# Performance work log

Measured on AMD Instinct MI355X. Metric: run time of the kernel, lower is better.

Reference implementation:

```python
import jax, jax.numpy as jnp
import numpy as np

B, S, D, H = 4, 2048, 1024, 16
HD = D // H
DFF = 4 * D
EPS = 1e-5


def gelu_tanh(x):
    c = jnp.sqrt(jnp.asarray(2.0 / jnp.pi, x.dtype))
    return 0.5 * x * (1.0 + jnp.tanh(c * (x + 0.044715 * x ** 3)))


def layernorm(x, scale, shift):
    mean = jnp.mean(x, axis=-1, keepdims=True)
    var = jnp.var(x, axis=-1, keepdims=True)  # unbiased=False
    return scale * (x - mean) * jax.lax.rsqrt(var + EPS) + shift


def setup_inputs() -> dict:
    key = jax.random.key(0)
    ks = jax.random.split(key, 12)
    s_in = 1.0 / np.sqrt(D)
    s_ff = 1.0 / np.sqrt(DFF)
    return {
        "x": jax.random.normal(ks[0], (B, S, D), jnp.float32),
        "Wq": jax.random.uniform(ks[1], (D, D), jnp.float32, -s_in, s_in),
        "Wk": jax.random.uniform(ks[2], (D, D), jnp.float32, -s_in, s_in),
        "Wv": jax.random.uniform(ks[3], (D, D), jnp.float32, -s_in, s_in),
        "Wo": jax.random.uniform(ks[4], (D, D), jnp.float32, -s_in, s_in),
        "bo": jax.random.uniform(ks[5], (D,), jnp.float32, -s_in, s_in),
        "W1": jax.random.uniform(ks[6], (D, DFF), jnp.float32, -s_in, s_in),
        "b1": jax.random.uniform(ks[7], (DFF,), jnp.float32, -s_in, s_in),
        "W2": jax.random.uniform(ks[8], (DFF, D), jnp.float32, -s_ff, s_ff),
        "b2": jax.random.uniform(ks[9], (D,), jnp.float32, -s_ff, s_ff),
        "ln1_scale": jnp.ones((D,), jnp.float32),
        "ln1_shift": jnp.zeros((D,), jnp.float32),
        "ln2_scale": jnp.ones((D,), jnp.float32),
        "ln2_shift": jnp.zeros((D,), jnp.float32),
    }


def reference(x, Wq, Wk, Wv, Wo, bo, W1, b1, W2, b2,
              ln1_scale, ln1_shift, ln2_scale, ln2_shift):
    # --- pre-LN causal MHA ---
    h = layernorm(x, ln1_scale, ln1_shift)
    q = (h @ Wq).reshape(B, S, H, HD).transpose(0, 2, 1, 3)  # [B,H,S,hd]
    k = (h @ Wk).reshape(B, S, H, HD).transpose(0, 2, 1, 3)
    v = (h @ Wv).reshape(B, S, H, HD).transpose(0, 2, 1, 3)
    scores = jnp.einsum('bhqd,bhkd->bhqk', q, k)
    causal = jnp.tril(jnp.ones((S, S), bool))  # mask strict upper triangle
    scores = jnp.where(causal, scores, -jnp.inf)
    attn = jax.nn.softmax(scores / np.sqrt(HD), axis=-1)
    ctx = jnp.einsum('bhqk,bhkd->bhqd', attn, v)
    ctx = ctx.transpose(0, 2, 1, 3).reshape(B, S, D)
    x = x + (ctx @ Wo + bo)
    # --- FFN ---
    h = layernorm(x, ln2_scale, ln2_shift)
    h = gelu_tanh(h @ W1 + b1) @ W2 + b2
    return x + h
```

## Files before the change

### kernel.cpp

```cpp
#include <hip/hip_runtime.h>
#include <math.h>

#define S_LEN  2048
#define DMODEL 1024
#define NHEAD  16
#define BATCH  4
#define NROWS  (BATCH*S_LEN)
#define DFF    4096
#define QKV_LD 3072

typedef __attribute__((ext_vector_type(4))) unsigned short us4;
typedef __attribute__((ext_vector_type(8))) unsigned short us8;
typedef __attribute__((ext_vector_type(8))) __bf16 bf16x8;
typedef __attribute__((ext_vector_type(4))) float f32x4;

#if __has_builtin(__builtin_amdgcn_exp2f)
#define EXP2(x) __builtin_amdgcn_exp2f(x)
#else
#define EXP2(x) exp2f(x)
#endif
#if __has_builtin(__builtin_amdgcn_rcpf)
#define RCP(x) __builtin_amdgcn_rcpf(x)
#else
#define RCP(x) (1.0f/(x))
#endif

static __device__ __forceinline__ unsigned short f2bf(float f) {
  __bf16 b = (__bf16)f;
  return __builtin_bit_cast(unsigned short, b);
}
#define GLD16(gp, lp) __builtin_amdgcn_global_load_lds( \
    (const __attribute__((address_space(1))) unsigned int*)(gp), \
    (__attribute__((address_space(3))) unsigned int*)(lp), 16, 0, 0)

static __device__ __forceinline__ int xcd_swz(int bid, int nwg) {
  int q = nwg >> 3;
  return (bid & 7) * q + (bid >> 3);
}

__global__ __launch_bounds__(256) void ln_kernel(
    const float* __restrict__ x, const float* __restrict__ scale,
    const float* __restrict__ shift, unsigned short* __restrict__ out)
{
  const int row = blockIdx.x, tid = threadIdx.x;
  const int lane = tid & 63, wave = tid >> 6;
  const float* xr = x + (size_t)row * DMODEL;
  f32x4 v = *(const f32x4*)&xr[tid * 4];
  float s  = v[0]+v[1]+v[2]+v[3];
  float s2 = v[0]*v[0]+v[1]*v[1]+v[2]*v[2]+v[3]*v[3];
  #pragma unroll
  for (int m = 1; m < 64; m <<= 1) { s += __shfl_xor(s, m); s2 += __shfl_xor(s2, m); }
  __shared__ float red[8];
  if (lane == 0) { red[wave] = s; red[4 + wave] = s2; }
  __syncthreads();
  s  = red[0]+red[1]+red[2]+red[3];
  s2 = red[4]+red[5]+red[6]+red[7];
  float mean = s * (1.0f/DMODEL);
  float var  = s2 * (1.0f/DMODEL) - mean*mean;
  float rstd = rsqrtf(var + 1e-5f);
  us4 o;
  #pragma unroll
  for (int j = 0; j < 4; j++) {
    float val = (v[j]-mean)*rstd*scale[tid*4+j] + shift[tid*4+j];
    o[j] = f2bf(val);
  }
  *(us4*)&out[(size_t)row*DMODEL + tid*4] = o;
}

__global__ __launch_bounds__(256) void wtrans_all(
    const float* __restrict__ Wq, const float* __restrict__ Wk,
    const float* __restrict__ Wv, const float* __restrict__ Wo,
    const float* __restrict__ W1, const float* __restrict__ W2,
    unsigned short* __restrict__ wqkvt, unsigned short* __restrict__ wot,
    unsigned short* __restrict__ w1t, unsigned short* __restrict__ w2t,
    float sclq)
{
  __shared__ unsigned short tile[64][72];
  const int bid = blockIdx.x, tid = threadIdx.x;
  const float* W; unsigned short* Wt; int K, N, sub; float scl = 1.0f;
  if (bid < 1024) {
    int wsel = bid >> 8; sub = bid & 255; K = 1024; N = 1024;
    W  = (wsel == 0) ? Wq : (wsel == 1) ? Wk : (wsel == 2) ? Wv : Wo;
    Wt = (wsel == 0) ? wqkvt : (wsel == 1) ? wqkvt + 1024*1024
       : (wsel == 2) ? wqkvt + 2048*1024 : wot;
    if (wsel == 0) scl = sclq;
  } else if (bid < 2048) { sub = bid - 1024; K = 1024; N = 4096; W = W1; Wt = w1t; }
  else                   { sub = bid - 2048; K = 4096; N = 1024; W = W2; Wt = w2t; }
  const int nbn = N >> 6;
  const int kt = sub / nbn, nt = sub % nbn;
  int r = tid >> 2, c0 = (tid & 3) << 4;
  const float* src = W + (size_t)(kt*64 + r)*N + nt*64 + c0;
  #pragma unroll
  for (int j = 0; j < 16; j += 4) {
    f32x4 f = *(const f32x4*)&src[j];
    tile[r][c0+j+0] = f2bf(f[0]*scl); tile[r][c0+j+1] = f2bf(f[1]*scl);
    tile[r][c0+j+2] = f2bf(f[2]*scl); tile[r][c0+j+3] = f2bf(f[3]*scl);
  }
  __syncthreads();
  int n = tid >> 2, k0 = (tid & 3) << 4;
  us8 o0, o1;
  #pragma unroll
  for (int j = 0; j < 8; j++) { o0[j] = tile[k0+j][n]; o1[j] = tile[k0+8+j][n]; }
  unsigned short* dst = Wt + (size_t)(nt*64 + n)*K + kt*64 + k0;
  *(us8*)&dst[0] = o0;
  *(us8*)&dst[8] = o1;
}

__global__ __launch_bounds__(256) void vtrans(
    const unsigned short* __restrict__ v, unsigned short* __restrict__ vt)
{
  __shared__ unsigned short tile[64][72];
  const int tid = threadIdx.x;
  const int bh = blockIdx.x >> 5, st = blockIdx.x & 31;
  const int b = bh >> 4, h = bh & 15;
  int r = tid >> 2, c0 = (tid & 3) << 4;
  const unsigned short* src = v + (size_t)(b*S_LEN + st*64 + r)*QKV_LD + h*64 + c0;
  *(us8*)&tile[r][c0]   = *(const us8*)&src[0];
  *(us8*)&tile[r][c0+8] = *(const us8*)&src[8];
  __syncthreads();
  int d = tid >> 2, s0 = (tid & 3) << 4;
  us8 o0, o1;
  #pragma unroll
  for (int j = 0; j < 8; j++) { o0[j] = tile[s0+j][d]; o1[j] = tile[s0+8+j][d]; }
  unsigned short* dst = vt + (size_t)(bh*64 + d)*S_LEN + st*64 + s0;
  *(us8*)&dst[0] = o0;
  *(us8*)&dst[8] = o1;
}

template<bool BIAS, bool GELU_>
__global__ __launch_bounds__(512, 2) void gemm256(
    const unsigned short* __restrict__ A, const unsigned short* __restrict__ Bt,
    unsigned short* __restrict__ Cout, const float* __restrict__ bias,
    int M, int N, int K)
{
  constexpr int BN = 256, WN = 64, NF = 4;
  __shared__ unsigned short sA[2][256*64];
  __shared__ unsigned short sB[2][BN*64];
  const int tid = threadIdx.x;
  const int wave = tid >> 6, lane = tid & 63;
  const int wm = wave >> 2, wn = wave & 3;
  const int l15 = lane & 15, g = lane >> 4, x7 = lane & 7, r8 = lane >> 3;
  const int srcc = (x7 ^ r8) << 3;
  const int nbn = N / BN;
  const int bid = xcd_swz(blockIdx.x, gridDim.x);
  const int bm = bid / nbn, bn = bid % nbn;
  const unsigned short* gA = A  + (size_t)(bm*256)*K;
  const unsigned short* gB = Bt + (size_t)(bn*BN)*K;
  const int NT = K >> 6;

  f32x4 acc[8][NF] = {};

#define STAGEA(buf, h, kb) do { \
    _Pragma("unroll") \
    for (int j_ = 0; j_ < 2; j_++) \
      GLD16(gA + (size_t)((h)*128 + j_*64 + wave*8 + r8)*K + (kb) + srcc, \
            &sA[buf][((h)*128 + j_*64 + wave*8)*64]); \
  } while (0)
#define STAGEB(buf, h, kb) do { \
    _Pragma("unroll") \
    for (int j_ = 0; j_ < 2; j_++) \
      GLD16(gB + (size_t)((h)*128 + j_*64 + wave*8 + r8)*K + (kb) + srcc, \
            &sB[buf][((h)*128 + j_*64 + wave*8)*64]); \
  } while (0)
#define RDA_(m, kk) (*(const bf16x8*)&cA[(wm*128 + (m)*16 + l15)*64 + ((((kk)*4+g)^x7)<<3)])
#define RDB_(n, kk) (*(const bf16x8*)&cB[(wn*WN + (n)*16 + l15)*64 + ((((kk)*4+g)^x7)<<3)])
#define PH(p) do { \
    __builtin_amdgcn_s_setprio(1); \
    _Pragma("unroll") for (int mm_ = 0; mm_ < 2; mm_++) \
    _Pragma("unroll") for (int n_ = 0; n_ < NF; n_++) \
    _Pragma("unroll") for (int kk_ = 0; kk_ < 2; kk_++) \
      acc[(p)*2+mm_][n_] = __builtin_amdgcn_mfma_f32_16x16x32_bf16( \
          af[mm_][kk_], bfr[n_][kk_], acc[(p)*2+mm_][n_], 0, 0, 0); \
    __builtin_amdgcn_s_setprio(0); \
  } while (0)

  STAGEB(0, 0, 0); STAGEB(0, 1, 0);
  STAGEA(0, 0, 0); STAGEA(0, 1, 0);
  STAGEB(1, 0, 64); STAGEB(1, 1, 64);

  for (int t = 0; t < NT; ++t) {
    const int c = t & 1;
    const unsigned short* cA = sA[c];
    const unsigned short* cB = sB[c];
    const int kb1 = (t + 1) * 64, kb2 = (t + 2) * 64;
    bf16x8 af[2][2], bfr[NF][2];

    if (t < NT - 1) asm volatile("s_waitcnt vmcnt(4)" ::: "memory");
    else            asm volatile("s_waitcnt vmcnt(0)" ::: "memory");
    __builtin_amdgcn_s_barrier();
    __builtin_amdgcn_sched_barrier(0);

    #pragma unroll
    for (int n = 0; n < NF; n++) { bfr[n][0] = RDB_(n, 0); bfr[n][1] = RDB_(n, 1); }
    af[0][0] = RDA_(0, 0); af[0][1] = RDA_(0, 1);
    af[1][0] = RDA_(1, 0); af[1][1] = RDA_(1, 1);
    if (t + 1 < NT) STAGEA(c ^ 1, 0, kb1);
    PH(0);
    af[0][0] = RDA_(2, 0); af[0][1] = RDA_(2, 1);
    af[1][0] = RDA_(3, 0); af[1][1] = RDA_(3, 1);
    if (t + 1 < NT) STAGEA(c ^ 1, 1, kb1);
    PH(1);
    __builtin_amdgcn_s_barrier();
    af[0][0] = RDA_(4, 0); af[0][1] = RDA_(4, 1);
    af[1][0] = RDA_(5, 0); af[1][1] = RDA_(5, 1);
    if (t + 2 < NT) STAGEB(c, 0, kb2);
    PH(2);
    af[0][0] = RDA_(6, 0); af[0][1] = RDA_(6, 1);
    af[1][0] = RDA_(7, 0); af[1][1] = RDA_(7, 1);
    if (t + 2 < NT) STAGEB(c, 1, kb2);
    PH(3);
  }

  #pragma unroll
  for (int m = 0; m < 8; m++) {
    #pragma unroll
    for (int r = 0; r < 4; r++) {
      int grow = bm*256 + wm*128 + m*16 + g*4 + r;
      #pragma unroll
      for (int n = 0; n < NF; n++) {
        int gcol = bn*BN + wn*WN + n*16 + l15;
        float v = acc[m][n][r];
        if (BIAS) v += bias[gcol];
        if (GELU_) {
          float xx = v;
          float u = 0.7978845608f*(xx + 0.044715f*xx*xx*xx);
          float e = EXP2(u * 2.88539008f);
          float th = 1.0f - 2.0f*RCP(e + 1.0f);
          v = 0.5f*xx*(1.0f + th);
        }
        Cout[(size_t)grow*N + gcol] = f2bf(v);
      }
    }
  }
#undef STAGEA
#undef STAGEB
#undef RDA_
#undef RDB_
#undef PH
}

template<bool BIAS, bool GELU_, bool RESID, bool OUTF32>
__global__ __launch_bounds__(512, 2) void gemm128(
    const unsigned short* __restrict__ A, const unsigned short* __restrict__ Bt,
    void* Cout, const float* __restrict__ bias, const float* resid,
    int M, int N, int K)
{
  __shared__ unsigned short sA[2][128*64];
  __shared__ unsigned short sB[2][256*64];
  const int tid = threadIdx.x;
  const int wave = tid >> 6, lane = tid & 63;
  const int wm = wave >> 2, wn = wave & 3;
  const int l15 = lane & 15, g = lane >> 4, x7 = lane & 7, r8 = lane >> 3;
  const int srcc = (x7 ^ r8) << 3;
  const int nbn = N >> 8;
  const int bid = xcd_swz(blockIdx.x, gridDim.x);
  const int bm = bid / nbn, bn = bid % nbn;
  const unsigned short* gA = A  + (size_t)(bm*128)*K;
  const unsigned short* gB = Bt + (size_t)(bn*256)*K;
  const int NT = K >> 6;

  f32x4 acc[4][4] = {};

#define STAGEA1(buf, kb) do { \
    _Pragma("unroll") \
    for (int j_ = 0; j_ < 2; j_++) \
      GLD16(gA + (size_t)(j_*64 + wave*8 + r8)*K + (kb) + srcc, \
            &sA[buf][(j_*64 + wave*8)*64]); \
  } while (0)
#define STAGEB1(buf, kb) do { \
    _Pragma("unroll") \
    for (int j_ = 0; j_ < 4; j_++) \
      GLD16(gB + (size_t)(j_*64 + wave*8 + r8)*K + (kb) + srcc, \
            &sB[buf][(j_*64 + wave*8)*64]); \
  } while (0)
#define RDA1(m, kk) (*(const bf16x8*)&cA[(wm*64 + (m)*16 + l15)*64 + ((((kk)*4+g)^x7)<<3)])
#define RDB1(n, kk) (*(const bf16x8*)&cB[(wn*64 + (n)*16 + l15)*64 + ((((kk)*4+g)^x7)<<3)])
#define PH1(p) do { \
    __builtin_amdgcn_s_setprio(1); \
    _Pragma("unroll") for (int mm_ = 0; mm_ < 2; mm_++) \
    _Pragma("unroll") for (int n_ = 0; n_ < 4; n_++) \
    _Pragma("unroll") for (int kk_ = 0; kk_ < 2; kk_++) \
      acc[(p)*2+mm_][n_] = __builtin_amdgcn_mfma_f32_16x16x32_bf16( \
          af[mm_][kk_], bfr[n_][kk_], acc[(p)*2+mm_][n_], 0, 0, 0); \
    __builtin_amdgcn_s_setprio(0); \
  } while (0)

  STAGEB1(0, 0);
  STAGEA1(0, 0);
  STAGEB1(1, 64);

  for (int t = 0; t < NT; ++t) {
    const int c = t & 1;
    const unsigned short* cA = sA[c];
    const unsigned short* cB = sB[c];
    const int kb1 = (t + 1) * 64, kb2 = (t + 2) * 64;
    bf16x8 af[2][2], bfr[4][2];

    if (t < NT - 1) asm volatile("s_waitcnt vmcnt(4)" ::: "memory");
    else            asm volatile("s_waitcnt vmcnt(0)" ::: "memory");
    __builtin_amdgcn_s_barrier();
    __builtin_amdgcn_sched_barrier(0);

    #pragma unroll
    for (int n = 0; n < 4; n++) { bfr[n][0] = RDB1(n, 0); bfr[n][1] = RDB1(n, 1); }
    af[0][0] = RDA1(0, 0); af[0][1] = RDA1(0, 1);
    af[1][0] = RDA1(1, 0); af[1][1] = RDA1(1, 1);
    if (t + 1 < NT) STAGEA1(c ^ 1, kb1);
    PH1(0);
    __builtin_amdgcn_s_barrier();
    af[0][0] = RDA1(2, 0); af[0][1] = RDA1(2, 1);
    af[1][0] = RDA1(3, 0); af[1][1] = RDA1(3, 1);
    if (t + 2 < NT) STAGEB1(c, kb2);
    PH1(1);
  }

  #pragma unroll
  for (int m = 0; m < 4; m++) {
    #pragma unroll
    for (int r = 0; r < 4; r++) {
      int grow = bm*128 + wm*64 + m*16 + g*4 + r;
      #pragma unroll
      for (int n = 0; n < 4; n++) {
        int gcol = bn*256 + wn*64 + n*16 + l15;
        float v = acc[m][n][r];
        if (BIAS) v += bias[gcol];
        if (GELU_) {
          float xx = v;
          float u = 0.7978845608f*(xx + 0.044715f*xx*xx*xx);
          float e = EXP2(u * 2.88539008f);
          float th = 1.0f - 2.0f*RCP(e + 1.0f);
          v = 0.5f*xx*(1.0f + th);
        }
        if (RESID) v += resid[(size_t)grow*N + gcol];
        if (OUTF32) ((float*)Cout)[(size_t)grow*N + gcol] = v;
        else ((unsigned short*)Cout)[(size_t)grow*N + gcol] = f2bf(v);
      }
    }
  }
#undef STAGEA1
#undef STAGEB1
#undef RDA1
#undef RDB1
#undef PH1
}

__global__ __launch_bounds__(512) void attn_kernel(
    const unsigned short* __restrict__ qb, const unsigned short* __restrict__ kb,
    const unsigned short* __restrict__ vt, unsigned short* __restrict__ ctx)
{
  __shared__ unsigned short sK[2][64*64];
  __shared__ unsigned short sV[2][64*64];
  __shared__ unsigned short sP[8][16*64];
  const int tid = threadIdx.x, wave = tid >> 6, lane = tid & 63;
  const int l15 = lane & 15, g = lane >> 4, x7 = lane & 7;
  const int qt = 15 - (blockIdx.x >> 6);
  const int bh = blockIdx.x & 63;
  const int b = bh >> 4, h = bh & 15;
  const int qrow = qt*128 + wave*16;
  const int NTI = 2*qt + 2;

  bf16x8 qf[2];
  {
    const unsigned short* qr = qb + (size_t)(b*S_LEN + qrow + l15) * QKV_LD + h*64;
    qf[0] = *(const bf16x8*)&qr[g*8];
    qf[1] = *(const bf16x8*)&qr[32 + g*8];
  }

  us8 ones_u;
  #pragma unroll
  for (int j = 0; j < 8; j++) ones_u[j] = 0x3F80;
  const bf16x8 ones8 = __builtin_bit_cast(bf16x8, ones_u);

  f32x4 oacc[4] = {};
  f32x4 lacc = {};
  float mrow[4];
  #pragma unroll
  for (int r = 0; r < 4; r++) mrow[r] = -INFINITY;

  const int rrow = lane >> 3;
  const int srcc = (x7 ^ rrow) << 3;
  const unsigned short* kbase = kb + (size_t)(b*S_LEN)*QKV_LD + h*64 + srcc;
  const unsigned short* vbase = vt + (size_t)(bh*64)*S_LEN + srcc;

#define ASTAGE(buf, t) do { \
    const int kv0_ = (t)*64; \
    GLD16(kbase + (size_t)(kv0_ + wave*8 + rrow)*QKV_LD, &sK[buf][wave*8*64]); \
    GLD16(vbase + (size_t)(wave*8 + rrow)*S_LEN + kv0_,  &sV[buf][wave*8*64]); \
  } while(0)

  ASTAGE(0, 0);

  for (int t = 0; t < NTI; ++t) {
    __syncthreads();
    const int cur = t & 1;
    if (t < NTI - 1) ASTAGE(cur ^ 1, t + 1);

    const int kv0 = t*64;
    if (kv0 > qrow + 15) continue;

    f32x4 sacc[4] = {};
    __builtin_amdgcn_s_setprio(1);
    #pragma unroll
    for (int kk = 0; kk < 2; kk++) {
      const int csw = ((kk*4 + g) ^ x7) << 3;
      #pragma unroll
      for (int n = 0; n < 4; n++) {
        bf16x8 kf = *(const bf16x8*)&sK[cur][(n*16 + l15)*64 + csw];
        sacc[n] = __builtin_amdgcn_mfma_f32_16x16x32_bf16(qf[kk], kf, sacc[n], 0, 0, 0);
      }
    }
    __builtin_amdgcn_s_setprio(0);

    float p[4][4], rm[4];
    const bool masked = (kv0 + 63 > qrow);
    #pragma unroll
    for (int r = 0; r < 4; r++) {
      float m_ = -INFINITY;
      #pragma unroll
      for (int n = 0; n < 4; n++) {
        float sc = sacc[n][r];
        if (masked && (kv0 + n*16 + l15) > (qrow + g*4 + r)) sc = -INFINITY;
        p[n][r] = sc;
        m_ = fmaxf(m_, sc);
      }
      rm[r] = m_;
    }
    bool need = (rm[0] > mrow[0] + 8.0f) | (rm[1] > mrow[1] + 8.0f) |
                (rm[2] > mrow[2] + 8.0f) | (rm[3] > mrow[3] + 8.0f);
    if (__any(need)) {
      #pragma unroll
      for (int r = 0; r < 4; r++) {
        float vv = rm[r];
        vv = fmaxf(vv, __shfl_xor(vv, 1));
        vv = fmaxf(vv, __shfl_xor(vv, 2));
        vv = fmaxf(vv, __shfl_xor(vv, 4));
        vv = fmaxf(vv, __shfl_xor(vv, 8));
        float mn = fmaxf(mrow[r], vv);
        float alpha = EXP2(mrow[r] - mn);
        mrow[r] = mn;
        lacc[r] *= alpha;
        #pragma unroll
        for (int nd = 0; nd < 4; nd++) oacc[nd][r] *= alpha;
      }
    }
    #pragma unroll
    for (int n = 0; n < 4; n++)
      #pragma unroll
      for (int r = 0; r < 4; r++)
        p[n][r] = EXP2(p[n][r] - mrow[r]);

    #pragma unroll
    for (int n = 0; n < 4; n++) {
      const int chunk = n*2 + (l15 >> 3);
      #pragma unroll
      for (int r = 0; r < 4; r++) {
        const int prow = g*4 + r;
        sP[wave][prow*64 + ((chunk ^ (prow & 7)) << 3) + x7] = f2bf(p[n][r]);
      }
    }
    asm volatile("s_waitcnt lgkmcnt(0)" ::: "memory");
    __builtin_amdgcn_sched_barrier(0);

    __builtin_amdgcn_s_setprio(1);
    #pragma unroll
    for (int kk = 0; kk < 2; kk++) {
      const int csw = ((kk*4 + g) ^ x7) << 3;
      bf16x8 pa = *(const bf16x8*)&sP[wave][l15*64 + csw];
      #pragma unroll
      for (int nd = 0; nd < 4; nd++) {
        bf16x8 vf = *(const bf16x8*)&sV[cur][(nd*16 + l15)*64 + csw];
        oacc[nd] = __builtin_amdgcn_mfma_f32_16x16x32_bf16(pa, vf, oacc[nd], 0, 0, 0);
      }
      lacc = __builtin_amdgcn_mfma_f32_16x16x32_bf16(pa, ones8, lacc, 0, 0, 0);
    }
    __builtin_amdgcn_s_setprio(0);
  }

  #pragma unroll
  for (int r = 0; r < 4; r++) {
    float inv = RCP(lacc[r]);
    size_t row = (size_t)(b*S_LEN + qrow + g*4 + r);
    #pragma unroll
    for (int nd = 0; nd < 4; nd++)
      ctx[row*DMODEL + h*64 + nd*16 + l15] = f2bf(oacc[nd][r] * inv);
  }
}

extern "C" void kernel_launch(void* const* d_in, const int* in_sizes, int n_in,
                              void* d_out, int out_size, void* d_ws, size_t ws_size,
                              hipStream_t stream)
{
  const float* x    = (const float*)d_in[0];
  const float* Wq   = (const float*)d_in[1];
  const float* Wk   = (const float*)d_in[2];
  const float* Wv   = (const float*)d_in[3];
  const float* Wo   = (const float*)d_in[4];
  const float* bo   = (const float*)d_in[5];
  const float* W1   = (const float*)d_in[6];
  const float* b1   = (const float*)d_in[7];
  const float* W2   = (const float*)d_in[8];
  const float* b2   = (const float*)d_in[9];
  const float* ln1s = (const float*)d_in[10];
  const float* ln1b = (const float*)d_in[11];
  const float* ln2s = (const float*)d_in[12];
  const float* ln2b = (const float*)d_in[13];
  float* out = (float*)d_out;
  (void)in_sizes; (void)n_in; (void)out_size; (void)ws_size;

  char* ws = (char*)d_ws;
  size_t off = 0;
  auto alloc = [&](size_t n) { char* p = ws + off; off += (n + 255) & ~(size_t)255; return p; };
  unsigned short* hbuf  = (unsigned short*)alloc((size_t)NROWS*DMODEL*2);
  unsigned short* qkv   = (unsigned short*)alloc((size_t)NROWS*QKV_LD*2);
  unsigned short* vtb   = (unsigned short*)alloc((size_t)NROWS*DMODEL*2);
  unsigned short* ctx   = (unsigned short*)alloc((size_t)NROWS*DMODEL*2);
  unsigned short* ffn1  = (unsigned short*)alloc((size_t)NROWS*DFF*2);
  unsigned short* wqkvt = (unsigned short*)alloc((size_t)QKV_LD*DMODEL*2);
  unsigned short* wot   = (unsigned short*)alloc((size_t)DMODEL*DMODEL*2);
  unsigned short* w1t   = (unsigned short*)alloc((size_t)DFF*DMODEL*2);
  unsigned short* w2t   = (unsigned short*)alloc((size_t)DMODEL*DFF*2);

  const float SCLQ = 0.18033688011f;

  wtrans_all<<<dim3(3072), dim3(256), 0, stream>>>(
      Wq, Wk, Wv, Wo, W1, W2, wqkvt, wot, w1t, w2t, SCLQ);

  ln_kernel<<<dim3(NROWS), dim3(256), 0, stream>>>(x, ln1s, ln1b, hbuf);
  gemm256<false,false><<<dim3(32*12), dim3(512), 0, stream>>>(
      hbuf, wqkvt, qkv, nullptr, NROWS, QKV_LD, DMODEL);
  vtrans<<<dim3(2048), dim3(256), 0, stream>>>(qkv + 2048, vtb);
  attn_kernel<<<dim3(1024), dim3(512), 0, stream>>>(qkv, qkv + 1024, vtb, ctx);
  gemm128<true,false,true,true><<<dim3(64*4), dim3(512), 0, stream>>>(
      ctx, wot, (void*)out, bo, x, NROWS, DMODEL, DMODEL);
  ln_kernel<<<dim3(NROWS), dim3(256), 0, stream>>>(out, ln2s, ln2b, hbuf);
  gemm256<true,true><<<dim3(32*16), dim3(512), 0, stream>>>(
      hbuf, w1t, ffn1, b1, NROWS, DFF, DMODEL);
  gemm128<true,false,true,true><<<dim3(64*4), dim3(512), 0, stream>>>(
      ffn1, w2t, (void*)out, b2, out, NROWS, DMODEL, DFF);
}
```

Before: 357.5 us.

## Replace 128x256 GEMM tile with 256x128 tile using four waves of 128x64

The output-projection and FFN2 GEMMs (N=1024) move from a 512-thread kernel with 128x256 tiles and 64x64 per-wave blocks to a 256-thread kernel with 256x128 tiles and 128x64 per-wave blocks. Each wave now holds twice as many accumulators, which raises MFMA work per LDS fragment load. Global staging is split into halves, spread across four compute phases per k-step. The cost is higher register pressure and fewer waves per block to hide latency, with the same grid of 256 blocks.

```diff
diff --git a/kernel.cpp b/kernel.cpp
--- a/kernel.cpp
+++ b/kernel.cpp
@@ -240,42 +240,42 @@
 }
 
 template<bool BIAS, bool GELU_, bool RESID, bool OUTF32>
-__global__ __launch_bounds__(512, 2) void gemm128(
+__global__ __launch_bounds__(256) void gemm_nk(
     const unsigned short* __restrict__ A, const unsigned short* __restrict__ Bt,
     void* Cout, const float* __restrict__ bias, const float* resid,
     int M, int N, int K)
 {
-  __shared__ unsigned short sA[2][128*64];
-  __shared__ unsigned short sB[2][256*64];
+  __shared__ unsigned short sA[2][256*64];
+  __shared__ unsigned short sB[2][128*64];
   const int tid = threadIdx.x;
   const int wave = tid >> 6, lane = tid & 63;
-  const int wm = wave >> 2, wn = wave & 3;
+  const int wm = wave >> 1, wn = wave & 1;
   const int l15 = lane & 15, g = lane >> 4, x7 = lane & 7, r8 = lane >> 3;
   const int srcc = (x7 ^ r8) << 3;
-  const int nbn = N >> 8;
+  const int nbn = N >> 7;
   const int bid = xcd_swz(blockIdx.x, gridDim.x);
   const int bm = bid / nbn, bn = bid % nbn;
-  const unsigned short* gA = A  + (size_t)(bm*128)*K;
-  const unsigned short* gB = Bt + (size_t)(bn*256)*K;
+  const unsigned short* gA = A  + (size_t)(bm*256)*K;
+  const unsigned short* gB = Bt + (size_t)(bn*128)*K;
   const int NT = K >> 6;
 
-  f32x4 acc[4][4] = {};
-
-#define STAGEA1(buf, kb) do { \
+  f32x4 acc[8][4] = {};
+
+#define STAGEA2(buf, h, kb) do { \
+    _Pragma("unroll") \
+    for (int j_ = 0; j_ < 4; j_++) \
+      GLD16(gA + (size_t)(wave*64 + (h)*32 + j_*8 + r8)*K + (kb) + srcc, \
+            &sA[buf][(wave*64 + (h)*32 + j_*8)*64]); \
+  } while (0)
+#define STAGEB2(buf, h, kb) do { \
     _Pragma("unroll") \
     for (int j_ = 0; j_ < 2; j_++) \
-      GLD16(gA + (size_t)(j_*64 + wave*8 + r8)*K + (kb) + srcc, \
-            &sA[buf][(j_*64 + wave*8)*64]); \
+      GLD16(gB + (size_t)(wave*32 + (h)*16 + j_*8 + r8)*K + (kb) + srcc, \
+            &sB[buf][(wave*32 + (h)*16 + j_*8)*64]); \
   } while (0)
-#define STAGEB1(buf, kb) do { \
-    _Pragma("unroll") \
-    for (int j_ = 0; j_ < 4; j_++) \
-      GLD16(gB + (size_t)(j_*64 + wave*8 + r8)*K + (kb) + srcc, \
-            &sB[buf][(j_*64 + wave*8)*64]); \
-  } while (0)
-#define RDA1(m, kk) (*(const bf16x8*)&cA[(wm*64 + (m)*16 + l15)*64 + ((((kk)*4+g)^x7)<<3)])
-#define RDB1(n, kk) (*(const bf16x8*)&cB[(wn*64 + (n)*16 + l15)*64 + ((((kk)*4+g)^x7)<<3)])
-#define PH1(p) do { \
+#define RDA2(m, kk) (*(const bf16x8*)&cA[(wm*128 + (m)*16 + l15)*64 + ((((kk)*4+g)^x7)<<3)])
+#define RDB2(n, kk) (*(const bf16x8*)&cB[(wn*64  + (n)*16 + l15)*64 + ((((kk)*4+g)^x7)<<3)])
+#define PH2(p) do { \
     __builtin_amdgcn_s_setprio(1); \
     _Pragma("unroll") for (int mm_ = 0; mm_ < 2; mm_++) \
     _Pragma("unroll") for (int n_ = 0; n_ < 4; n_++) \
@@ -285,9 +285,9 @@
     __builtin_amdgcn_s_setprio(0); \
   } while (0)
 
-  STAGEB1(0, 0);
-  STAGEA1(0, 0);
-  STAGEB1(1, 64);
+  STAGEB2(0, 0, 0); STAGEB2(0, 1, 0);
+  STAGEA2(0, 0, 0); STAGEA2(0, 1, 0);
+  STAGEB2(1, 0, 64); STAGEB2(1, 1, 64);
 
   for (int t = 0; t < NT; ++t) {
     const int c = t & 1;
@@ -302,26 +302,34 @@
     __builtin_amdgcn_sched_barrier(0);
 
     #pragma unroll
-    for (int n = 0; n < 4; n++) { bfr[n][0] = RDB1(n, 0); bfr[n][1] = RDB1(n, 1); }
-    af[0][0] = RDA1(0, 0); af[0][1] = RDA1(0, 1);
-    af[1][0] = RDA1(1, 0); af[1][1] = RDA1(1, 1);
-    if (t + 1 < NT) STAGEA1(c ^ 1, kb1);
-    PH1(0);
+    for (int n = 0; n < 4; n++) { bfr[n][0] = RDB2(n, 0); bfr[n][1] = RDB2(n, 1); }
+    af[0][0] = RDA2(0, 0); af[0][1] = RDA2(0, 1);
+    af[1][0] = RDA2(1, 0); af[1][1] = RDA2(1, 1);
+    if (t + 1 < NT) STAGEA2(c ^ 1, 0, kb1);
+    PH2(0);
     __builtin_amdgcn_s_barrier();
-    af[0][0] = RDA1(2, 0); af[0][1] = RDA1(2, 1);
-    af[1][0] = RDA1(3, 0); af[1][1] = RDA1(3, 1);
-    if (t + 2 < NT) STAGEB1(c, kb2);
-    PH1(1);
-  }
-
-  #pragma unroll
-  for (int m = 0; m < 4; m++) {
+    af[0][0] = RDA2(2, 0); af[0][1] = RDA2(2, 1);
+    af[1][0] = RDA2(3, 0); af[1][1] = RDA2(3, 1);
+    if (t + 1 < NT) STAGEA2(c ^ 1, 1, kb1);
+    PH2(1);
+    af[0][0] = RDA2(4, 0); af[0][1] = RDA2(4, 1);
+    af[1][0] = RDA2(5, 0); af[1][1] = RDA2(5, 1);
+    if (t + 2 < NT) STAGEB2(c, 0, kb2);
+    PH2(2);
+    af[0][0] = RDA2(6, 0); af[0][1] = RDA2(6, 1);
+    af[1][0] = RDA2(7, 0); af[1][1] = RDA2(7, 1);
+    if (t + 2 < NT) STAGEB2(c, 1, kb2);
+    PH2(3);
+  }
+
+  #pragma unroll
+  for (int m = 0; m < 8; m++) {
     #pragma unroll
     for (int r = 0; r < 4; r++) {
-      int grow = bm*128 + wm*64 + m*16 + g*4 + r;
+      int grow = bm*256 + wm*128 + m*16 + g*4 + r;
       #pragma unroll
       for (int n = 0; n < 4; n++) {
-        int gcol = bn*256 + wn*64 + n*16 + l15;
+        int gcol = bn*128 + wn*64 + n*16 + l15;
         float v = acc[m][n][r];
         if (BIAS) v += bias[gcol];
         if (GELU_) {
@@ -337,11 +345,11 @@
       }
     }
   }
-#undef STAGEA1
-#undef STAGEB1
-#undef RDA1
-#undef RDB1
-#undef PH1
+#undef STAGEA2
+#undef STAGEB2
+#undef RDA2
+#undef RDB2
+#undef PH2
 }
 
 __global__ __launch_bounds__(512) void attn_kernel(
@@ -530,11 +538,11 @@
       hbuf, wqkvt, qkv, nullptr, NROWS, QKV_LD, DMODEL);
   vtrans<<<dim3(2048), dim3(256), 0, stream>>>(qkv + 2048, vtb);
   attn_kernel<<<dim3(1024), dim3(512), 0, stream>>>(qkv, qkv + 1024, vtb, ctx);
-  gemm128<true,false,true,true><<<dim3(64*4), dim3(512), 0, stream>>>(
+  gemm_nk<true,false,true,true><<<dim3(32*8), dim3(256), 0, stream>>>(
       ctx, wot, (void*)out, bo, x, NROWS, DMODEL, DMODEL);
   ln_kernel<<<dim3(NROWS), dim3(256), 0, stream>>>(out, ln2s, ln2b, hbuf);
   gemm256<true,true><<<dim3(32*16), dim3(512), 0, stream>>>(
       hbuf, w1t, ffn1, b1, NROWS, DFF, DMODEL);
-  gemm128<true,false,true,true><<<dim3(64*4), dim3(512), 0, stream>>>(
+  gemm_nk<true,false,true,true><<<dim3(32*8), dim3(256), 0, stream>>>(
       ffn1, w2t, (void*)out, b2, out, NROWS, DMODEL, DFF);
 }
```

Result: slower. 404.2 us (+13.1%).

## Split-K the FFN2 GEMM with 256x256 tiles plus a separate reduce kernel

Applied to the files above, without the earlier changes.

The FFN down-projection (K=4096) moves from a 128x256-tile GEMM with a fused bias/residual epilogue to a 256x256-tile GEMM that splits K in two. Each half writes fp32 partial sums into the dead qkv/vtb workspace. A new elementwise kernel then adds both partials, the bias and the residual into the output. The larger tile is meant to improve operand reuse per block while keeping the grid at 256 blocks. In exchange it adds roughly 64 MB of fp32 partial writes and reads plus an extra kernel launch.

```diff
diff --git a/kernel.cpp b/kernel.cpp
--- a/kernel.cpp
+++ b/kernel.cpp
@@ -239,6 +239,123 @@
 #undef PH
 }
 
+__global__ __launch_bounds__(512, 2) void gemm256sk(
+    const unsigned short* __restrict__ A, const unsigned short* __restrict__ Bt,
+    float* __restrict__ P,
+    int M, int N, int K)
+{
+  __shared__ unsigned short sA[2][256*64];
+  __shared__ unsigned short sB[2][256*64];
+  const int tid = threadIdx.x;
+  const int wave = tid >> 6, lane = tid & 63;
+  const int wm = wave >> 2, wn = wave & 3;
+  const int l15 = lane & 15, g = lane >> 4, x7 = lane & 7, r8 = lane >> 3;
+  const int srcc = (x7 ^ r8) << 3;
+  const int nbn = N >> 8;
+  const int bid = xcd_swz(blockIdx.x, gridDim.x);
+  const int bn = bid % nbn;
+  const int ks = (bid / nbn) & 1;
+  const int bm = bid / (nbn * 2);
+  const int KH = K >> 1;
+  const unsigned short* gA = A  + (size_t)(bm*256)*K + ks*KH;
+  const unsigned short* gB = Bt + (size_t)(bn*256)*K + ks*KH;
+  float* Pout = P + (size_t)ks * M * N;
+  const int NT = KH >> 6;
+
+  f32x4 acc[8][4] = {};
+
+#define SKA(buf, h, kb) do { \
+    _Pragma("unroll") \
+    for (int j_ = 0; j_ < 2; j_++) \
+      GLD16(gA + (size_t)((h)*128 + j_*64 + wave*8 + r8)*K + (kb) + srcc, \
+            &sA[buf][((h)*128 + j_*64 + wave*8)*64]); \
+  } while (0)
+#define SKB(buf, h, kb) do { \
+    _Pragma("unroll") \
+    for (int j_ = 0; j_ < 2; j_++) \
+      GLD16(gB + (size_t)((h)*128 + j_*64 + wave*8 + r8)*K + (kb) + srcc, \
+            &sB[buf][((h)*128 + j_*64 + wave*8)*64]); \
+  } while (0)
+#define SRA(m, kk) (*(const bf16x8*)&cA[(wm*128 + (m)*16 + l15)*64 + ((((kk)*4+g)^x7)<<3)])
+#define SRB(n, kk) (*(const bf16x8*)&cB[(wn*64  + (n)*16 + l15)*64 + ((((kk)*4+g)^x7)<<3)])
+#define SPH(p) do { \
+    __builtin_amdgcn_s_setprio(1); \
+    _Pragma("unroll") for (int mm_ = 0; mm_ < 2; mm_++) \
+    _Pragma("unroll") for (int n_ = 0; n_ < 4; n_++) \
+    _Pragma("unroll") for (int kk_ = 0; kk_ < 2; kk_++) \
+      acc[(p)*2+mm_][n_] = __builtin_amdgcn_mfma_f32_16x16x32_bf16( \
+          af[mm_][kk_], bfr[n_][kk_], acc[(p)*2+mm_][n_], 0, 0, 0); \
+    __builtin_amdgcn_s_setprio(0); \
+  } while (0)
+
+  SKB(0, 0, 0); SKB(0, 1, 0);
+  SKA(0, 0, 0); SKA(0, 1, 0);
+  SKB(1, 0, 64); SKB(1, 1, 64);
+
+  for (int t = 0; t < NT; ++t) {
+    const int c = t & 1;
+    const unsigned short* cA = sA[c];
+    const unsigned short* cB = sB[c];
+    const int kb1 = (t + 1) * 64, kb2 = (t + 2) * 64;
+    bf16x8 af[2][2], bfr[4][2];
+
+    if (t < NT - 1) asm volatile("s_waitcnt vmcnt(4)" ::: "memory");
+    else            asm volatile("s_waitcnt vmcnt(0)" ::: "memory");
+    __builtin_amdgcn_s_barrier();
+    __builtin_amdgcn_sched_barrier(0);
+
+    #pragma unroll
+    for (int n = 0; n < 4; n++) { bfr[n][0] = SRB(n, 0); bfr[n][1] = SRB(n, 1); }
+    af[0][0] = SRA(0, 0); af[0][1] = SRA(0, 1);
+    af[1][0] = SRA(1, 0); af[1][1] = SRA(1, 1);
+    if (t + 1 < NT) SKA(c ^ 1, 0, kb1);
+    SPH(0);
+    af[0][0] = SRA(2, 0); af[0][1] = SRA(2, 1);
+    af[1][0] = SRA(3, 0); af[1][1] = SRA(3, 1);
+    if (t + 1 < NT) SKA(c ^ 1, 1, kb1);
+    SPH(1);
+    __builtin_amdgcn_s_barrier();
+    af[0][0] = SRA(4, 0); af[0][1] = SRA(4, 1);
+    af[1][0] = SRA(5, 0); af[1][1] = SRA(5, 1);
+    if (t + 2 < NT) SKB(c, 0, kb2);
+    SPH(2);
+    af[0][0] = SRA(6, 0); af[0][1] = SRA(6, 1);
+    af[1][0] = SRA(7, 0); af[1][1] = SRA(7, 1);
+    if (t + 2 < NT) SKB(c, 1, kb2);
+    SPH(3);
+  }
+
+  #pragma unroll
+  for (int m = 0; m < 8; m++)
+    #pragma unroll
+    for (int r = 0; r < 4; r++) {
+      int grow = bm*256 + wm*128 + m*16 + g*4 + r;
+      #pragma unroll
+      for (int n = 0; n < 4; n++)
+        Pout[(size_t)grow*N + bn*256 + wn*64 + n*16 + l15] = acc[m][n][r];
+    }
+#undef SKA
+#undef SKB
+#undef SRA
+#undef SRB
+#undef SPH
+}
+
+__global__ __launch_bounds__(256) void ffn2_reduce(
+    const float* __restrict__ p, const float* __restrict__ bias,
+    float* __restrict__ out)
+{
+  const int row = blockIdx.x, tid = threadIdx.x;
+  const size_t i = (size_t)row * DMODEL + tid * 4;
+  f32x4 a = *(const f32x4*)&p[i];
+  f32x4 b = *(const f32x4*)&p[(size_t)NROWS * DMODEL + i];
+  f32x4 o = *(const f32x4*)&out[i];
+  f32x4 bb = *(const f32x4*)&bias[tid * 4];
+  #pragma unroll
+  for (int j = 0; j < 4; j++) o[j] += a[j] + b[j] + bb[j];
+  *(f32x4*)&out[i] = o;
+}
+
 template<bool BIAS, bool GELU_, bool RESID, bool OUTF32>
 __global__ __launch_bounds__(512, 2) void gemm128(
     const unsigned short* __restrict__ A, const unsigned short* __restrict__ Bt,
@@ -519,6 +636,7 @@
   unsigned short* wot   = (unsigned short*)alloc((size_t)DMODEL*DMODEL*2);
   unsigned short* w1t   = (unsigned short*)alloc((size_t)DFF*DMODEL*2);
   unsigned short* w2t   = (unsigned short*)alloc((size_t)DMODEL*DFF*2);
+  float* psum = (float*)qkv;
 
   const float SCLQ = 0.18033688011f;
 
@@ -535,6 +653,7 @@
   ln_kernel<<<dim3(NROWS), dim3(256), 0, stream>>>(out, ln2s, ln2b, hbuf);
   gemm256<true,true><<<dim3(32*16), dim3(512), 0, stream>>>(
       hbuf, w1t, ffn1, b1, NROWS, DFF, DMODEL);
-  gemm128<true,false,true,true><<<dim3(64*4), dim3(512), 0, stream>>>(
-      ffn1, w2t, (void*)out, b2, out, NROWS, DMODEL, DFF);
-}
+  gemm256sk<<<dim3(32*4*2), dim3(512), 0, stream>>>(
+      ffn1, w2t, psum, NROWS, DMODEL, DFF);
+  ffn2_reduce<<<dim3(NROWS), dim3(256), 0, stream>>>(psum, b2, out);
+}
```

Measured after the change: 361.5 us. Within noise of the previous version (+1.1%).

## Reschedule 256x256 GEMM pipeline and split-K the FFN2 GEMM with a reduce kernel

Applied to the files above, without the earlier changes.

Replaces the 256x256 bf16 GEMM main loop with a four-phase schedule. Each phase has explicit barriers, an lgkmcnt wait and incremented global pointers for staging A and B, and occupancy drops to one block per CU. The FFN down-projection moves from the 128-row GEMM to a 2-way split-K 256x256 GEMM that writes fp32 partials into the reused qkv buffer. A separate reduce kernel then adds both partials, the bias and the residual. This aims to raise MFMA utilisation and fill the GPU for the K=4096 GEMM, at the cost of extra fp32 partial traffic and one more launch.

```diff
diff --git a/kernel.cpp b/kernel.cpp
--- a/kernel.cpp
+++ b/kernel.cpp
@@ -127,89 +127,96 @@
   *(us8*)&dst[8] = o1;
 }
 
-template<bool BIAS, bool GELU_>
-__global__ __launch_bounds__(512, 2) void gemm256(
-    const unsigned short* __restrict__ A, const unsigned short* __restrict__ Bt,
-    unsigned short* __restrict__ Cout, const float* __restrict__ bias,
-    int M, int N, int K)
-{
-  constexpr int BN = 256, WN = 64, NF = 4;
-  __shared__ unsigned short sA[2][256*64];
-  __shared__ unsigned short sB[2][BN*64];
-  const int tid = threadIdx.x;
-  const int wave = tid >> 6, lane = tid & 63;
-  const int wm = wave >> 2, wn = wave & 3;
-  const int l15 = lane & 15, g = lane >> 4, x7 = lane & 7, r8 = lane >> 3;
+#define G8_IDS \
+  const int tid = threadIdx.x; \
+  const int wave = tid >> 6, lane = tid & 63; \
+  const int wm = wave >> 2, wn = wave & 3; \
+  const int l15 = lane & 15, g = lane >> 4, x7 = lane & 7, r8 = lane >> 3; \
   const int srcc = (x7 ^ r8) << 3;
-  const int nbn = N / BN;
-  const int bid = xcd_swz(blockIdx.x, gridDim.x);
-  const int bm = bid / nbn, bn = bid % nbn;
-  const unsigned short* gA = A  + (size_t)(bm*256)*K;
-  const unsigned short* gB = Bt + (size_t)(bn*BN)*K;
-  const int NT = K >> 6;
-
-  f32x4 acc[8][NF] = {};
-
-#define STAGEA(buf, h, kb) do { \
-    _Pragma("unroll") \
-    for (int j_ = 0; j_ < 2; j_++) \
-      GLD16(gA + (size_t)((h)*128 + j_*64 + wave*8 + r8)*K + (kb) + srcc, \
-            &sA[buf][((h)*128 + j_*64 + wave*8)*64]); \
-  } while (0)
-#define STAGEB(buf, h, kb) do { \
-    _Pragma("unroll") \
-    for (int j_ = 0; j_ < 2; j_++) \
-      GLD16(gB + (size_t)((h)*128 + j_*64 + wave*8 + r8)*K + (kb) + srcc, \
-            &sB[buf][((h)*128 + j_*64 + wave*8)*64]); \
-  } while (0)
+
 #define RDA_(m, kk) (*(const bf16x8*)&cA[(wm*128 + (m)*16 + l15)*64 + ((((kk)*4+g)^x7)<<3)])
-#define RDB_(n, kk) (*(const bf16x8*)&cB[(wn*WN + (n)*16 + l15)*64 + ((((kk)*4+g)^x7)<<3)])
-#define PH(p) do { \
+#define RDB_(n, kk) (*(const bf16x8*)&cB[(wn*64  + (n)*16 + l15)*64 + ((((kk)*4+g)^x7)<<3)])
+#define READ_B() do { _Pragma("unroll") \
+    for (int n_ = 0; n_ < 4; n_++) { bfr[n_][0] = RDB_(n_, 0); bfr[n_][1] = RDB_(n_, 1); } } while (0)
+#define READ_A(m0_) do { \
+    af[0][0] = RDA_(m0_, 0);   af[0][1] = RDA_(m0_, 1); \
+    af[1][0] = RDA_(m0_+1, 0); af[1][1] = RDA_(m0_+1, 1); } while (0)
+#define MF16(p) do { \
     __builtin_amdgcn_s_setprio(1); \
     _Pragma("unroll") for (int mm_ = 0; mm_ < 2; mm_++) \
-    _Pragma("unroll") for (int n_ = 0; n_ < NF; n_++) \
+    _Pragma("unroll") for (int n_ = 0; n_ < 4; n_++) \
     _Pragma("unroll") for (int kk_ = 0; kk_ < 2; kk_++) \
       acc[(p)*2+mm_][n_] = __builtin_amdgcn_mfma_f32_16x16x32_bf16( \
           af[mm_][kk_], bfr[n_][kk_], acc[(p)*2+mm_][n_], 0, 0, 0); \
     __builtin_amdgcn_s_setprio(0); \
   } while (0)
-
-  STAGEB(0, 0, 0); STAGEB(0, 1, 0);
-  STAGEA(0, 0, 0); STAGEA(0, 1, 0);
-  STAGEB(1, 0, 64); STAGEB(1, 1, 64);
-
-  for (int t = 0; t < NT; ++t) {
-    const int c = t & 1;
-    const unsigned short* cA = sA[c];
-    const unsigned short* cB = sB[c];
-    const int kb1 = (t + 1) * 64, kb2 = (t + 2) * 64;
-    bf16x8 af[2][2], bfr[NF][2];
-
-    if (t < NT - 1) asm volatile("s_waitcnt vmcnt(4)" ::: "memory");
-    else            asm volatile("s_waitcnt vmcnt(0)" ::: "memory");
-    __builtin_amdgcn_s_barrier();
-    __builtin_amdgcn_sched_barrier(0);
-
-    #pragma unroll
-    for (int n = 0; n < NF; n++) { bfr[n][0] = RDB_(n, 0); bfr[n][1] = RDB_(n, 1); }
-    af[0][0] = RDA_(0, 0); af[0][1] = RDA_(0, 1);
-    af[1][0] = RDA_(1, 0); af[1][1] = RDA_(1, 1);
-    if (t + 1 < NT) STAGEA(c ^ 1, 0, kb1);
-    PH(0);
-    af[0][0] = RDA_(2, 0); af[0][1] = RDA_(2, 1);
-    af[1][0] = RDA_(3, 0); af[1][1] = RDA_(3, 1);
-    if (t + 1 < NT) STAGEA(c ^ 1, 1, kb1);
-    PH(1);
-    __builtin_amdgcn_s_barrier();
-    af[0][0] = RDA_(4, 0); af[0][1] = RDA_(4, 1);
-    af[1][0] = RDA_(5, 0); af[1][1] = RDA_(5, 1);
-    if (t + 2 < NT) STAGEB(c, 0, kb2);
-    PH(2);
-    af[0][0] = RDA_(6, 0); af[0][1] = RDA_(6, 1);
-    af[1][0] = RDA_(7, 0); af[1][1] = RDA_(7, 1);
-    if (t + 2 < NT) STAGEB(c, 1, kb2);
-    PH(3);
-  }
+#define STG(ptr, smat, nb, ubase) do { \
+    GLD16(ptr, &smat[nb][((ubase) + wave*8)*64]); ptr += 64; } while (0)
+#define BARR  __builtin_amdgcn_s_barrier(); __builtin_amdgcn_sched_barrier(0)
+#define LGKM0 asm volatile("s_waitcnt lgkmcnt(0)" ::: "memory"); __builtin_amdgcn_sched_barrier(0)
+#define VM(n) asm volatile("s_waitcnt vmcnt(" #n ")" ::: "memory")
+
+#define G8_LOOP(NT) \
+  for (int t = 0; t < (NT); ++t) { \
+    const int c = t & 1, nb = c ^ 1; \
+    const unsigned short* cA = sA[c]; \
+    const unsigned short* cB = sB[c]; \
+    const bool pf = (t + 1 < (NT)); \
+    bf16x8 af[2][2], bfr[4][2]; \
+     \
+    READ_B(); READ_A(0); \
+    if (pf) { STG(pB0, sB, nb, 0); STG(pB1, sB, nb, 64); } \
+    BARR; LGKM0; MF16(0); BARR; \
+     \
+    READ_A(2); \
+    if (pf) { STG(pB2, sB, nb, 128); STG(pB3, sB, nb, 192); } \
+    if (pf) { VM(4); } else { VM(0); } \
+    BARR; LGKM0; MF16(1); BARR; \
+     \
+    READ_A(4); \
+    if (pf) { STG(pA0, sA, nb, 0); STG(pA2, sA, nb, 128); } \
+    BARR; LGKM0; MF16(2); BARR; \
+     \
+    READ_A(6); \
+    if (pf) { STG(pA1, sA, nb, 64); STG(pA3, sA, nb, 192); } \
+    if (pf) { VM(2); } \
+    BARR; LGKM0; MF16(3); BARR; \
+  }
+
+#define G8_PROLOGUE \
+  STG(pB0, sB, 0, 0); STG(pB1, sB, 0, 64); STG(pB2, sB, 0, 128); STG(pB3, sB, 0, 192); \
+  STG(pA0, sA, 0, 0); STG(pA2, sA, 0, 128); STG(pA1, sA, 0, 64); STG(pA3, sA, 0, 192); \
+  VM(2); __builtin_amdgcn_s_barrier(); __builtin_amdgcn_sched_barrier(0)
+
+template<bool BIAS, bool GELU_>
+__global__ __launch_bounds__(512, 1) void gemm256p(
+    const unsigned short* __restrict__ A, const unsigned short* __restrict__ Bt,
+    unsigned short* __restrict__ Cout, const float* __restrict__ bias,
+    int M, int N, int K)
+{
+  __shared__ unsigned short sA[2][256*64];
+  __shared__ unsigned short sB[2][256*64];
+  G8_IDS;
+  const int nbn = N >> 8;
+  const int bid = xcd_swz(blockIdx.x, gridDim.x);
+  const int bm = bid / nbn, bn = bid % nbn;
+  const unsigned short* gA = A  + (size_t)(bm*256)*K;
+  const unsigned short* gB = Bt + (size_t)(bn*256)*K;
+  const int NT = K >> 6;
+
+  f32x4 acc[8][4] = {};
+  const int trow = wave*8 + r8;
+  const unsigned short* pB0 = gB + (size_t)(trow +   0)*K + srcc;
+  const unsigned short* pB1 = gB + (size_t)(trow +  64)*K + srcc;
+  const unsigned short* pB2 = gB + (size_t)(trow + 128)*K + srcc;
+  const unsigned short* pB3 = gB + (size_t)(trow + 192)*K + srcc;
+  const unsigned short* pA0 = gA + (size_t)(trow +   0)*K + srcc;
+  const unsigned short* pA1 = gA + (size_t)(trow +  64)*K + srcc;
+  const unsigned short* pA2 = gA + (size_t)(trow + 128)*K + srcc;
+  const unsigned short* pA3 = gA + (size_t)(trow + 192)*K + srcc;
+
+  G8_PROLOGUE;
+  G8_LOOP(NT);
 
   #pragma unroll
   for (int m = 0; m < 8; m++) {
@@ -217,8 +224,8 @@
     for (int r = 0; r < 4; r++) {
       int grow = bm*256 + wm*128 + m*16 + g*4 + r;
       #pragma unroll
-      for (int n = 0; n < NF; n++) {
-        int gcol = bn*BN + wn*WN + n*16 + l15;
+      for (int n = 0; n < 4; n++) {
+        int gcol = bn*256 + wn*64 + n*16 + l15;
         float v = acc[m][n][r];
         if (BIAS) v += bias[gcol];
         if (GELU_) {
@@ -232,11 +239,64 @@
       }
     }
   }
-#undef STAGEA
-#undef STAGEB
-#undef RDA_
-#undef RDB_
-#undef PH
+}
+
+__global__ __launch_bounds__(512, 1) void gemm256skp(
+    const unsigned short* __restrict__ A, const unsigned short* __restrict__ Bt,
+    float* __restrict__ P, int M, int N, int K)
+{
+  __shared__ unsigned short sA[2][256*64];
+  __shared__ unsigned short sB[2][256*64];
+  G8_IDS;
+  const int nbn = N >> 8;
+  const int bid = xcd_swz(blockIdx.x, gridDim.x);
+  const int bn = bid % nbn;
+  const int ks = (bid / nbn) & 1;
+  const int bm = bid / (nbn * 2);
+  const int KH = K >> 1;
+  const unsigned short* gA = A  + (size_t)(bm*256)*K + ks*KH;
+  const unsigned short* gB = Bt + (size_t)(bn*256)*K + ks*KH;
+  float* Pout = P + (size_t)ks * M * N;
+  const int NT = KH >> 6;
+
+  f32x4 acc[8][4] = {};
+  const int trow = wave*8 + r8;
+  const unsigned short* pB0 = gB + (size_t)(trow +   0)*K + srcc;
+  const unsigned short* pB1 = gB + (size_t)(trow +  64)*K + srcc;
+  const unsigned short* pB2 = gB + (size_t)(trow + 128)*K + srcc;
+  const unsigned short* pB3 = gB + (size_t)(trow + 192)*K + srcc;
+  const unsigned short* pA0 = gA + (size_t)(trow +   0)*K + srcc;
+  const unsigned short* pA1 = gA + (size_t)(trow +  64)*K + srcc;
+  const unsigned short* pA2 = gA + (size_t)(trow + 128)*K + srcc;
+  const unsigned short* pA3 = gA + (size_t)(trow + 192)*K + srcc;
+
+  G8_PROLOGUE;
+  G8_LOOP(NT);
+
+  #pragma unroll
+  for (int m = 0; m < 8; m++)
+    #pragma unroll
+    for (int r = 0; r < 4; r++) {
+      int grow = bm*256 + wm*128 + m*16 + g*4 + r;
+      #pragma unroll
+      for (int n = 0; n < 4; n++)
+        Pout[(size_t)grow*N + bn*256 + wn*64 + n*16 + l15] = acc[m][n][r];
+    }
+}
+
+__global__ __launch_bounds__(256) void ffn2_reduce(
+    const float* __restrict__ p, const float* __restrict__ bias,
+    float* __restrict__ out)
+{
+  const int row = blockIdx.x, tid = threadIdx.x;
+  const size_t i = (size_t)row * DMODEL + tid * 4;
+  f32x4 a = *(const f32x4*)&p[i];
+  f32x4 b = *(const f32x4*)&p[(size_t)NROWS * DMODEL + i];
+  f32x4 o = *(const f32x4*)&out[i];
+  f32x4 bb = *(const f32x4*)&bias[tid * 4];
+  #pragma unroll
+  for (int j = 0; j < 4; j++) o[j] += a[j] + b[j] + bb[j];
+  *(f32x4*)&out[i] = o;
 }
 
 template<bool BIAS, bool GELU_, bool RESID, bool OUTF32>
@@ -519,6 +579,7 @@
   unsigned short* wot   = (unsigned short*)alloc((size_t)DMODEL*DMODEL*2);
   unsigned short* w1t   = (unsigned short*)alloc((size_t)DFF*DMODEL*2);
   unsigned short* w2t   = (unsigned short*)alloc((size_t)DMODEL*DFF*2);
+  float* psum = (float*)qkv;
 
   const float SCLQ = 0.18033688011f;
 
@@ -526,15 +587,16 @@
       Wq, Wk, Wv, Wo, W1, W2, wqkvt, wot, w1t, w2t, SCLQ);
 
   ln_kernel<<<dim3(NROWS), dim3(256), 0, stream>>>(x, ln1s, ln1b, hbuf);
-  gemm256<false,false><<<dim3(32*12), dim3(512), 0, stream>>>(
+  gemm256p<false,false><<<dim3(32*12), dim3(512), 0, stream>>>(
       hbuf, wqkvt, qkv, nullptr, NROWS, QKV_LD, DMODEL);
   vtrans<<<dim3(2048), dim3(256), 0, stream>>>(qkv + 2048, vtb);
   attn_kernel<<<dim3(1024), dim3(512), 0, stream>>>(qkv, qkv + 1024, vtb, ctx);
   gemm128<true,false,true,true><<<dim3(64*4), dim3(512), 0, stream>>>(
       ctx, wot, (void*)out, bo, x, NROWS, DMODEL, DMODEL);
   ln_kernel<<<dim3(NROWS), dim3(256), 0, stream>>>(out, ln2s, ln2b, hbuf);
-  gemm256<true,true><<<dim3(32*16), dim3(512), 0, stream>>>(
+  gemm256p<true,true><<<dim3(32*16), dim3(512), 0, stream>>>(
       hbuf, w1t, ffn1, b1, NROWS, DFF, DMODEL);
-  gemm128<true,false,true,true><<<dim3(64*4), dim3(512), 0, stream>>>(
-      ffn1, w2t, (void*)out, b2, out, NROWS, DMODEL, DFF);
-}
+  gemm256skp<<<dim3(32*4*2), dim3(512), 0, stream>>>(
+      ffn1, w2t, psum, NROWS, DMODEL, DFF);
+  ffn2_reduce<<<dim3(NROWS), dim3(256), 0, stream>>>(psum, b2, out);
+}
```

Result: slower. 374.3 us (+4.7%).
